# Performance work log

Measured on AMD Instinct MI355X. Metric: run time of the kernel, lower is better.

Reference implementation:

```python
import jax, jax.numpy as jnp
import numpy as np

B, S, D = 2, 2048, 1024
H = 16
DK = D // H
LW = 256          # local window size
GSTRIDE = 64      # global downsample stride
SW = 512          # sliding window size
EPS = 1e-5
SCALE = 1.0 / np.sqrt(DK)


def _layernorm(x, g, b):
    mu = jnp.mean(x, axis=-1, keepdims=True)
    var = jnp.mean(jnp.square(x - mu), axis=-1, keepdims=True)
    return (x - mu) * jax.lax.rsqrt(var + EPS) * g + b


def setup_inputs() -> dict:
    key = jax.random.key(0)
    ks = jax.random.split(key, 16)
    std = 0.02
    def lin(k, din, dout):
        kw, kb = jax.random.split(k)
        return (jax.random.normal(kw, (din, dout), jnp.float32) * std,
                jax.random.normal(kb, (dout,), jnp.float32) * std)
    inp = {}
    inp["x"] = jax.random.normal(ks[0], (B, S, D), jnp.float32)
    # hierarchical attention params
    inp["lq_w"], inp["lq_b"] = lin(ks[1], D, D)
    inp["lk_w"], inp["lk_b"] = lin(ks[2], D, D)
    inp["lv_w"], inp["lv_b"] = lin(ks[3], D, D)
    inp["gq_w"], inp["gq_b"] = lin(ks[4], D, D)
    inp["gk_w"], inp["gk_b"] = lin(ks[5], D, D)
    inp["gv_w"], inp["gv_b"] = lin(ks[6], D, D)
    inp["h_out_w"], inp["h_out_b"] = lin(ks[7], 2 * D, D)
    inp["h_ln_g"] = jnp.ones((D,), jnp.float32)
    inp["h_ln_b"] = jnp.zeros((D,), jnp.float32)
    # sliding window attention params
    inp["sq_w"], inp["sq_b"] = lin(ks[8], D, D)
    inp["sk_w"], inp["sk_b"] = lin(ks[9], D, D)
    inp["sv_w"], inp["sv_b"] = lin(ks[10], D, D)
    inp["s_out_w"], inp["s_out_b"] = lin(ks[11], D, D)
    # combination
    inp["comb_w"], inp["comb_b"] = lin(ks[12], 2 * D, D)
    inp["ln_g"] = jnp.ones((D,), jnp.float32)
    inp["ln_b"] = jnp.zeros((D,), jnp.float32)
    return inp


def _forward(x, lq_w, lq_b, lk_w, lk_b, lv_w, lv_b,
             gq_w, gq_b, gk_w, gk_b, gv_w, gv_b,
             h_out_w, h_out_b, h_ln_g, h_ln_b,
             sq_w, sq_b, sk_w, sk_b, sv_w, sv_b,
             s_out_w, s_out_b, comb_w, comb_b, ln_g, ln_b):
    nw = S // LW  # seq_len is a multiple of LW (no padding needed)

    # ---- Hierarchical: local windowed attention (vectorized over windows) ----
    xw = x.reshape(B, nw, LW, D)
    lq = (xw @ lq_w + lq_b).reshape(B, nw, LW, H, DK)
    lk = (xw @ lk_w + lk_b).reshape(B, nw, LW, H, DK)
    lv = (xw @ lv_w + lv_b).reshape(B, nw, LW, H, DK)
    lsc = jnp.einsum('bnqhd,bnkhd->bnhqk', lq, lk) * SCALE
    lat = jax.nn.softmax(lsc, axis=-1)
    local_out = jnp.einsum('bnhqk,bnkhd->bnqhd', lat, lv).reshape(B, S, D)

    # ---- Hierarchical: global attention over strided downsample ----
    gc = x[:, ::GSTRIDE]                 # [B, G, D], G = S // GSTRIDE
    G = gc.shape[1]
    gq = (x @ gq_w + gq_b).reshape(B, S, H, DK)
    gk = (gc @ gk_w + gk_b).reshape(B, G, H, DK)
    gv = (gc @ gv_w + gv_b).reshape(B, G, H, DK)
    gsc = jnp.einsum('bqhd,bkhd->bhqk', gq, gk) * SCALE
    gat = jax.nn.softmax(gsc, axis=-1)
    global_out = jnp.einsum('bhqk,bkhd->bqhd', gat, gv).reshape(B, S, D)

    h_comb = jnp.concatenate([local_out, global_out], axis=-1) @ h_out_w + h_out_b
    h_out = _layernorm(x + h_comb, h_ln_g, h_ln_b)

    # ---- Sliding window attention ----
    sq = (x @ sq_w + sq_b).reshape(B, S, H, DK)
    sk = (x @ sk_w + sk_b).reshape(B, S, H, DK)
    sv = (x @ sv_w + sv_b).reshape(B, S, H, DK)
    ssc = jnp.einsum('bqhd,bkhd->bhqk', sq, sk) * SCALE
    idx = jnp.arange(S)
    half = SW // 2
    band = jnp.abs(idx[:, None] - idx[None, :]) <= half   # [S, S]
    ssc = jnp.where(band[None, None], ssc, -jnp.inf)
    sat = jax.nn.softmax(ssc, axis=-1)
    s_attn = jnp.einsum('bhqk,bkhd->bqhd', sat, sv).reshape(B, S, D)
    s_out = s_attn @ s_out_w + s_out_b

    # ---- combine scales ----
    combined = jnp.concatenate([h_out, s_out], axis=-1) @ comb_w + comb_b
    return _layernorm(x + combined, ln_g, ln_b)


def reference(x, lq_w, lq_b, lk_w, lk_b, lv_w, lv_b,
              gq_w, gq_b, gk_w, gk_b, gv_w, gv_b,
              h_out_w, h_out_b, h_ln_g, h_ln_b,
              sq_w, sq_b, sk_w, sk_b, sv_w, sv_b,
              s_out_w, s_out_b, comb_w, comb_b, ln_g, ln_b):
    return _forward(x, lq_w, lq_b, lk_w, lk_b, lv_w, lv_b,
                    gq_w, gq_b, gk_w, gk_b, gv_w, gv_b,
                    h_out_w, h_out_b, h_ln_g, h_ln_b,
                    sq_w, sq_b, sk_w, sk_b, sv_w, sv_b,
                    s_out_w, s_out_b, comb_w, comb_b, ln_g, ln_b)
```

## Files before the change

kernel.cpp:

```cpp
#include <hip/hip_runtime.h>

#define BATCH 2
#define SEQ   2048
#define DIM   1024
#define NH    16
#define DK    64
#define SCALE_F 0.125f
#define MASKED  -2e30f
#define MINIT   -1e30f

typedef __attribute__((ext_vector_type(4))) float f4;
typedef __attribute__((ext_vector_type(4))) float f32x4;
typedef __attribute__((ext_vector_type(8))) short s16x8;
typedef __attribute__((ext_vector_type(4))) int  i32x4;
typedef __attribute__((ext_vector_type(4))) unsigned short u16x4;

__device__ __forceinline__ float bf2f(unsigned short u){ return __uint_as_float(((unsigned)u) << 16); }
__device__ __forceinline__ unsigned short f2bf(float f){
  unsigned u = __float_as_uint(f);
  u += 0x7FFFu + ((u >> 16) & 1u);
  return (unsigned short)(u >> 16);
}

#define ASYNC_LDS16(g, l) \
  __builtin_amdgcn_global_load_lds((const __attribute__((address_space(1))) void*)(g), \
                                   (__attribute__((address_space(3))) void*)(l), 16, 0, 0)

__global__ __launch_bounds__(256) void cast_bf16_kernel(const float* __restrict__ in,
                                                        unsigned short* __restrict__ out, int n){
  int i = (blockIdx.x * 256 + threadIdx.x) * 4;
  if (i < n){
    f4 v = *(const f4*)&in[i];
    u16x4 o = { f2bf(v[0]), f2bf(v[1]), f2bf(v[2]), f2bf(v[3]) };
    *(u16x4*)&out[i] = o;
  }
}

struct TCP { const float* w[12]; unsigned short* wt[12]; };
__global__ __launch_bounds__(256) void transpose_cast_b(TCP P, int K){
  const float* W = P.w[blockIdx.z];
  unsigned short* Wt = P.wt[blockIdx.z];
  __shared__ float tile[32][33];
  int x = threadIdx.x & 31, y = threadIdx.x >> 5;
  int bc = blockIdx.x << 5;
  int br = blockIdx.y << 5;
  #pragma unroll
  for (int yy = y; yy < 32; yy += 8)
    tile[yy][x] = W[(size_t)(br + yy) * DIM + bc + x];
  __syncthreads();
  #pragma unroll
  for (int yy = y; yy < 32; yy += 8)
    Wt[(size_t)(bc + yy) * K + br + x] = f2bf(tile[x][yy]);
}

__global__ __launch_bounds__(256) void gc_extract(const float* __restrict__ x,
                                                  unsigned short* __restrict__ gcb){
  int row = blockIdx.x;
  int t = threadIdx.x;
  unsigned short* dst = gcb + (size_t)row * DIM;
  if (row < BATCH * 32){
    int b = row >> 5, g = row & 31;
    const float* src = x + ((size_t)b * SEQ + (size_t)g * 64) * DIM;
    f4 v = *(const f4*)&src[t * 4];
    u16x4 o = { f2bf(v[0]), f2bf(v[1]), f2bf(v[2]), f2bf(v[3]) };
    *(u16x4*)&dst[t * 4] = o;
  } else {
    u16x4 z = { 0, 0, 0, 0 };
    *(u16x4*)&dst[t * 4] = z;
  }
}

struct GOut { unsigned short* ob; float* of; const float* bias; int ld; int tr; };
struct GOuts { GOut d[4]; };

template<int BN>
__global__ __launch_bounds__(256) void gemm_bf16(
    const unsigned short* __restrict__ A, const unsigned short* __restrict__ Bt,
    GOuts descs, int K)
{
  constexpr int NF = BN / 32;
  __shared__ __align__(16) unsigned short As[128 * 32];
  __shared__ __align__(16) unsigned short Bs[BN * 32];
  const int tid = threadIdx.x;
  const int lane = tid & 63;
  const int w = tid >> 6;
  const int wr = w >> 1, wc = w & 1;
  const int gx = gridDim.x;
  const int nwg = gx * gridDim.y;
  const int orig = blockIdx.y * gx + blockIdx.x;
  const int swz = (orig & 7) * (nwg >> 3) + (orig >> 3);
  const int tx = swz % gx, ty = swz / gx;
  const int tm = ty << 7, tn = tx * BN;
  const GOut dsc = descs.d[tn >> 10];
  const int trans = dsc.tr;

  const int r0 = tid >> 2;
  const int c0 = (tid & 3) << 3;
  const unsigned short* Ag0 = A + (size_t)(tm + r0) * K + c0;
  const unsigned short* Ag1 = A + (size_t)(tm + r0 + 64) * K + c0;
  const unsigned short* Bg0 = Bt + (size_t)(tn + r0) * K + c0;
  const unsigned short* Bg1 = Bt + (size_t)(tn + (BN == 128 ? r0 + 64 : r0)) * K + c0;
  unsigned short* AsW0 = &As[w * 512];
  unsigned short* AsW1 = &As[w * 512 + 2048];
  unsigned short* BsW0 = &Bs[w * 512];
  unsigned short* BsW1 = &Bs[(BN == 128 ? w * 512 + 2048 : w * 512)];

  f32x4 acc[4][NF];
  #pragma unroll
  for (int m = 0; m < 4; ++m)
    #pragma unroll
    for (int n = 0; n < NF; ++n) acc[m][n] = (f32x4){0.f, 0.f, 0.f, 0.f};

  const int fr = lane & 15, fg = lane >> 4;
  for (int kk = 0; kk < K; kk += 32){
    ASYNC_LDS16(Ag0 + kk, AsW0);
    ASYNC_LDS16(Ag1 + kk, AsW1);
    ASYNC_LDS16(Bg0 + kk, BsW0);
    if constexpr (BN == 128) ASYNC_LDS16(Bg1 + kk, BsW1);
    __syncthreads();
    s16x8 af[4], bfv[NF];
    #pragma unroll
    for (int m = 0; m < 4; ++m)
      af[m] = *(const s16x8*)&As[(wr * 64 + m * 16 + fr) * 32 + fg * 8];
    #pragma unroll
    for (int n = 0; n < NF; ++n)
      bfv[n] = *(const s16x8*)&Bs[(wc * (BN / 2) + n * 16 + fr) * 32 + fg * 8];
    if (trans){
      #pragma unroll
      for (int m = 0; m < 4; ++m)
        #pragma unroll
        for (int n = 0; n < NF; ++n)
          acc[m][n] = __builtin_amdgcn_mfma_f32_16x16x32_bf16(bfv[n], af[m], acc[m][n], 0, 0, 0);
    } else {
      #pragma unroll
      for (int m = 0; m < 4; ++m)
        #pragma unroll
        for (int n = 0; n < NF; ++n)
          acc[m][n] = __builtin_amdgcn_mfma_f32_16x16x32_bf16(af[m], bfv[n], acc[m][n], 0, 0, 0);
    }
    __syncthreads();
  }
  #pragma unroll
  for (int m = 0; m < 4; ++m){
    #pragma unroll
    for (int n = 0; n < NF; ++n){
      if (!trans){
        int cl = (tn + wc * (BN / 2) + n * 16 + fr) & 1023;
        float bv = dsc.bias ? dsc.bias[cl] : 0.f;
        #pragma unroll
        for (int r = 0; r < 4; ++r){
          int row = tm + wr * 64 + m * 16 + fg * 4 + r;
          float v = acc[m][n][r] + bv;
          if (dsc.of) dsc.of[(size_t)row * dsc.ld + cl] = v;
          if (dsc.ob) dsc.ob[(size_t)row * dsc.ld + cl] = f2bf(v);
        }
      } else {
        int colT = tm + wr * 64 + m * 16 + fr;
        #pragma unroll
        for (int r = 0; r < 4; ++r){
          int dl = (tn + wc * (BN / 2) + n * 16 + fg * 4 + r) & 1023;
          float v = acc[m][n][r] + (dsc.bias ? dsc.bias[dl] : 0.f);
          dsc.ob[(size_t)dl * dsc.ld + colT] = f2bf(v);
        }
      }
    }
  }
}

template<int MODE>
__global__ __launch_bounds__(256) void mfma_attn(
    const unsigned short* __restrict__ Qb,
    const unsigned short* __restrict__ Kb,
    const unsigned short* __restrict__ Vtb, int ldvt,
    unsigned short* __restrict__ Out, int ldo, int ocol)
{
  __shared__ __align__(16) unsigned short Ks[64][72];
  __shared__ __align__(16) unsigned short Vs[64][72];
  __shared__ __align__(16) unsigned short Pl[4][16][72];
  const int tid = threadIdx.x, lane = tid & 63, wv = tid >> 6;
  const int fr = lane & 15, fg = lane >> 4;
  const int blk = blockIdx.x;
  const int h  = blk & 15;
  const int qc = (blk >> 4) & 31;
  const int b  = blk >> 9;
  const int q0 = qc * 64;
  const int tq0 = b * SEQ + q0;
  int jlo, ntile;
  if (MODE == 0){ jlo = (qc >> 2) << 8; ntile = 4; }
  else if (MODE == 1){
    jlo = q0 - 256 < 0 ? 0 : q0 - 256;
    int jhi = q0 + 320 > SEQ ? SEQ : q0 + 320;
    ntile = (jhi - jlo) >> 6;
  } else { jlo = 0; ntile = 1; }
  const int ktok0 = (MODE == 2) ? b * 32 : b * SEQ;

  s16x8 qf[2];
  {
    const size_t qrow = (size_t)(tq0 + wv * 16 + fr) * DIM + h * DK;
    qf[0] = *(const s16x8*)&Qb[qrow + fg * 8];
    qf[1] = *(const s16x8*)&Qb[qrow + 32 + fg * 8];
  }
  f32x4 of[4];
  #pragma unroll
  for (int dt = 0; dt < 4; ++dt) of[dt] = (f32x4){0.f, 0.f, 0.f, 0.f};
  f32x4 m4 = (f32x4){MINIT, MINIT, MINIT, MINIT};
  f32x4 l4 = (f32x4){0.f, 0.f, 0.f, 0.f};

  for (int t = 0; t < ntile; ++t){
    const int jb = jlo + t * 64;
    __syncthreads();
    #pragma unroll
    for (int p = 0; p < 2; ++p){
      int idx = p * 256 + tid;
      int row = idx >> 3, c8 = idx & 7;
      *(i32x4*)&Ks[row][c8 * 8] =
          *(const i32x4*)&Kb[(size_t)(ktok0 + jb + row) * DIM + h * DK + c8 * 8];
      i32x4 v = *(const i32x4*)&Vtb[(size_t)(h * DK + row) * ldvt + ktok0 + jb + c8 * 8];
      *(i32x4*)((char*)Vs + row * 144 + ((c8 * 16) ^ ((row & 7) << 4))) = v;
    }
    __syncthreads();
    f32x4 sf[4];
    #pragma unroll
    for (int t16 = 0; t16 < 4; ++t16){
      sf[t16] = (f32x4){0.f, 0.f, 0.f, 0.f};
      #pragma unroll
      for (int ks = 0; ks < 2; ++ks){
        s16x8 kf = *(const s16x8*)&Ks[t16 * 16 + fr][ks * 32 + fg * 8];
        sf[t16] = __builtin_amdgcn_mfma_f32_16x16x32_bf16(qf[ks], kf, sf[t16], 0, 0, 0);
      }
    }
    #pragma unroll
    for (int t16 = 0; t16 < 4; ++t16){
      int j = jb + t16 * 16 + fr;
      #pragma unroll
      for (int r = 0; r < 4; ++r){
        float v = sf[t16][r] * SCALE_F;
        bool valid = true;
        if (MODE == 1){ int dq = (q0 + wv * 16 + fg * 4 + r) - j; valid = (dq <= 256) && (dq >= -256); }
        if (MODE == 2){ valid = j < 32; }
        sf[t16][r] = valid ? v : MASKED;
      }
    }
    f32x4 mx;
    #pragma unroll
    for (int r = 0; r < 4; ++r)
      mx[r] = fmaxf(fmaxf(sf[0][r], sf[1][r]), fmaxf(sf[2][r], sf[3][r]));
    #pragma unroll
    for (int off = 1; off < 16; off <<= 1){
      #pragma unroll
      for (int r = 0; r < 4; ++r) mx[r] = fmaxf(mx[r], __shfl_xor(mx[r], off));
    }
    f32x4 sc;
    #pragma unroll
    for (int r = 0; r < 4; ++r){
      float mn = fmaxf(m4[r], mx[r]);
      sc[r] = __expf(m4[r] - mn);
      m4[r] = mn;
    }
    f32x4 sm = (f32x4){0.f, 0.f, 0.f, 0.f};
    #pragma unroll
    for (int t16 = 0; t16 < 4; ++t16){
      #pragma unroll
      for (int r = 0; r < 4; ++r){
        float e = __expf(sf[t16][r] - m4[r]);
        sm[r] += e;
        Pl[wv][fg * 4 + r][t16 * 16 + fr] = f2bf(e);
      }
    }
    #pragma unroll
    for (int off = 1; off < 16; off <<= 1){
      #pragma unroll
      for (int r = 0; r < 4; ++r) sm[r] += __shfl_xor(sm[r], off);
    }
    #pragma unroll
    for (int r = 0; r < 4; ++r) l4[r] = l4[r] * sc[r] + sm[r];
    #pragma unroll
    for (int dt = 0; dt < 4; ++dt)
      #pragma unroll
      for (int r = 0; r < 4; ++r) of[dt][r] *= sc[r];
    #pragma unroll
    for (int ks2 = 0; ks2 < 2; ++ks2){
      s16x8 pa = *(const s16x8*)&Pl[wv][fr][ks2 * 32 + fg * 8];
      #pragma unroll
      for (int dt = 0; dt < 4; ++dt){
        int d = dt * 16 + fr;
        s16x8 vf = *(const s16x8*)((char*)Vs + d * 144 + ((ks2 * 64 + fg * 16) ^ ((d & 7) << 4)));
        of[dt] = __builtin_amdgcn_mfma_f32_16x16x32_bf16(pa, vf, of[dt], 0, 0, 0);
      }
    }
  }
  #pragma unroll
  for (int dt = 0; dt < 4; ++dt){
    #pragma unroll
    for (int r = 0; r < 4; ++r){
      float val = of[dt][r] / l4[r];
      int q = tq0 + wv * 16 + fg * 4 + r;
      Out[(size_t)q * ldo + ocol + h * DK + dt * 16 + fr] = f2bf(val);
    }
  }
}

__global__ __launch_bounds__(256) void ln_fused(
    const float* __restrict__ x, const float* __restrict__ dlt,
    const float* __restrict__ g, const float* __restrict__ bta,
    float* __restrict__ outf, unsigned short* __restrict__ outb, int ldo)
{
  const int row = blockIdx.x;
  const int t = threadIdx.x, lane = t & 63, wv = t >> 6;
  const float* xr = x + (size_t)row * DIM;
  const float* dr = dlt + (size_t)row * DIM;
  f4 xv = *(const f4*)&xr[t * 4];
  f4 dv = *(const f4*)&dr[t * 4];
  f4 y = xv + dv;
  float s = y[0] + y[1] + y[2] + y[3];
  float ss = y[0]*y[0] + y[1]*y[1] + y[2]*y[2] + y[3]*y[3];
  #pragma unroll
  for (int off = 1; off < 64; off <<= 1){ s += __shfl_xor(s, off); ss += __shfl_xor(ss, off); }
  __shared__ float red[8];
  if (lane == 0){ red[wv] = s; red[wv + 4] = ss; }
  __syncthreads();
  float S = red[0] + red[1] + red[2] + red[3];
  float SS = red[4] + red[5] + red[6] + red[7];
  float mu = S * (1.f / DIM);
  float var = SS * (1.f / DIM) - mu * mu;
  float rs = rsqrtf(var + 1e-5f);
  f4 gv = *(const f4*)&g[t * 4];
  f4 bv = *(const f4*)&bta[t * 4];
  f4 o;
  #pragma unroll
  for (int i = 0; i < 4; ++i) o[i] = (y[i] - mu) * rs * gv[i] + bv[i];
  if (outf) *(f4*)&outf[(size_t)row * ldo + t * 4] = o;
  if (outb){
    u16x4 ob = { f2bf(o[0]), f2bf(o[1]), f2bf(o[2]), f2bf(o[3]) };
    *(u16x4*)&outb[(size_t)row * ldo + t * 4] = ob;
  }
}

extern "C" void kernel_launch(void* const* d_in, const int* in_sizes, int n_in,
                              void* d_out, int out_size, void* d_ws, size_t ws_size,
                              hipStream_t stream){
  (void)in_sizes; (void)n_in; (void)out_size; (void)ws_size;
  const float* x      = (const float*)d_in[0];
  const float* lq_w   = (const float*)d_in[1];  const float* lq_b  = (const float*)d_in[2];
  const float* lk_w   = (const float*)d_in[3];  const float* lk_b  = (const float*)d_in[4];
  const float* lv_w   = (const float*)d_in[5];  const float* lv_b  = (const float*)d_in[6];
  const float* gq_w   = (const float*)d_in[7];  const float* gq_b  = (const float*)d_in[8];
  const float* gk_w   = (const float*)d_in[9];  const float* gk_b  = (const float*)d_in[10];
  const float* gv_w   = (const float*)d_in[11]; const float* gv_b  = (const float*)d_in[12];
  const float* ho_w   = (const float*)d_in[13]; const float* ho_b  = (const float*)d_in[14];
  const float* hln_g  = (const float*)d_in[15]; const float* hln_b = (const float*)d_in[16];
  const float* sq_w   = (const float*)d_in[17]; const float* sq_b  = (const float*)d_in[18];
  const float* sk_w   = (const float*)d_in[19]; const float* sk_b  = (const float*)d_in[20];
  const float* sv_w   = (const float*)d_in[21]; const float* sv_b  = (const float*)d_in[22];
  const float* so_w   = (const float*)d_in[23]; const float* so_b  = (const float*)d_in[24];
  const float* cb_w   = (const float*)d_in[25]; const float* cb_b  = (const float*)d_in[26];
  const float* ln_g   = (const float*)d_in[27]; const float* ln_b  = (const float*)d_in[28];

  const size_t M = (size_t)BATCH * SEQ;
  const size_t W1 = (size_t)DIM * DIM;
  char* ws = (char*)d_ws;
  size_t off = 0;
  auto alloc = [&](size_t bytes) -> void* {
    void* p = ws + off; off += (bytes + 255) & ~(size_t)255; return p;
  };
  unsigned short* xb    = (unsigned short*)alloc(M * DIM * 2);
  unsigned short* wt_s  = (unsigned short*)alloc(3 * W1 * 2);
  unsigned short* wt_lg = (unsigned short*)alloc(4 * W1 * 2);
  unsigned short* wt_g2 = (unsigned short*)alloc(2 * W1 * 2);
  unsigned short* wt_so = (unsigned short*)alloc(W1 * 2);
  unsigned short* wt_ho = (unsigned short*)alloc(2 * W1 * 2);
  unsigned short* wt_cb = (unsigned short*)alloc(2 * W1 * 2);
  unsigned short* gcb   = (unsigned short*)alloc((size_t)128 * DIM * 2);
  unsigned short* qb    = (unsigned short*)alloc(M * DIM * 2);
  unsigned short* kb    = (unsigned short*)alloc(M * DIM * 2);
  unsigned short* vtb   = (unsigned short*)alloc(M * DIM * 2);
  unsigned short* qg    = (unsigned short*)alloc(M * DIM * 2);
  unsigned short* gkb   = (unsigned short*)alloc((size_t)128 * DIM * 2);
  unsigned short* vtg   = (unsigned short*)alloc((size_t)128 * DIM * 2);
  unsigned short* satt  = (unsigned short*)alloc(M * DIM * 2);
  unsigned short* hcat  = (unsigned short*)alloc(M * 2 * DIM * 2);
  unsigned short* ccat  = (unsigned short*)alloc(M * 2 * DIM * 2);
  float* Af             = (float*)alloc(M * DIM * 4);

  dim3 b256(256);
  cast_bf16_kernel<<<dim3((M * DIM) / 1024), b256, 0, stream>>>(x, xb, (int)(M * DIM));
  {
    TCP p1 = {};
    const float* ws_[10] = {sq_w, sk_w, sv_w, lq_w, lk_w, lv_w, gq_w, gk_w, gv_w, so_w};
    unsigned short* wts_[10] = {wt_s, wt_s + W1, wt_s + 2 * W1,
                                wt_lg, wt_lg + W1, wt_lg + 2 * W1, wt_lg + 3 * W1,
                                wt_g2, wt_g2 + W1, wt_so};
    for (int i = 0; i < 10; ++i){ p1.w[i] = ws_[i]; p1.wt[i] = wts_[i]; }
    transpose_cast_b<<<dim3(32, 32, 10), b256, 0, stream>>>(p1, DIM);
    TCP p2 = {};
    p2.w[0] = ho_w; p2.wt[0] = wt_ho;
    p2.w[1] = cb_w; p2.wt[1] = wt_cb;
    transpose_cast_b<<<dim3(32, 64, 2), b256, 0, stream>>>(p2, 2 * DIM);
  }
  gc_extract<<<dim3(128), b256, 0, stream>>>(x, gcb);

  dim3 attn_grid(1024);
  auto mk = [&](unsigned short* ob, float* of, const float* bias, int ld, int tr) -> GOut {
    GOut g; g.ob = ob; g.of = of; g.bias = bias; g.ld = ld; g.tr = tr; return g;
  };

  {
    GOuts ds = {};
    ds.d[0] = mk(qb,  nullptr, sq_b, DIM, 0);
    ds.d[1] = mk(kb,  nullptr, sk_b, DIM, 0);
    ds.d[2] = mk(vtb, nullptr, sv_b, (int)M, 1);
    gemm_bf16<128><<<dim3(24, 32), b256, 0, stream>>>(xb, wt_s, ds, DIM);
  }
  mfma_attn<1><<<attn_grid, b256, 0, stream>>>(qb, kb, vtb, (int)M, satt, DIM, 0);

  {
    GOuts ds = {};
    ds.d[0] = mk(qb,  nullptr, lq_b, DIM, 0);
    ds.d[1] = mk(kb,  nullptr, lk_b, DIM, 0);
    ds.d[2] = mk(vtb, nullptr, lv_b, (int)M, 1);
    ds.d[3] = mk(qg,  nullptr, gq_b, DIM, 0);
    gemm_bf16<128><<<dim3(32, 32), b256, 0, stream>>>(xb, wt_lg, ds, DIM);
  }
  {
    GOuts ds = {};
    ds.d[0] = mk(ccat + 1024, nullptr, so_b, 2 * DIM, 0);
    gemm_bf16<64><<<dim3(16, 32), b256, 0, stream>>>(satt, wt_so, ds, DIM);
  }
  mfma_attn<0><<<attn_grid, b256, 0, stream>>>(qb, kb, vtb, (int)M, hcat, 2 * DIM, 0);

  {
    GOuts ds = {};
    ds.d[0] = mk(gkb, nullptr, gk_b, DIM, 0);
    ds.d[1] = mk(vtg, nullptr, gv_b, 128, 1);
    gemm_bf16<128><<<dim3(16, 1), b256, 0, stream>>>(gcb, wt_g2, ds, DIM);
  }
  mfma_attn<2><<<attn_grid, b256, 0, stream>>>(qg, gkb, vtg, 128, hcat, 2 * DIM, 1024);

  {
    GOuts ds = {};
    ds.d[0] = mk(nullptr, Af, ho_b, DIM, 0);
    gemm_bf16<64><<<dim3(16, 32), b256, 0, stream>>>(hcat, wt_ho, ds, 2 * DIM);
  }
  ln_fused<<<dim3((int)M), b256, 0, stream>>>(x, Af, hln_g, hln_b, nullptr, ccat, 2 * DIM);

  {
    GOuts ds = {};
    ds.d[0] = mk(nullptr, Af, cb_b, DIM, 0);
    gemm_bf16<64><<<dim3(16, 32), b256, 0, stream>>>(ccat, wt_cb, ds, 2 * DIM);
  }
  ln_fused<<<dim3((int)M), b256, 0, stream>>>(x, Af, ln_g, ln_b, (float*)d_out, nullptr, DIM);
}
```

Baseline: 565.2 us.

## Double-buffer GEMM LDS tiles with async prefetch and XOR-swizzled layout

The bf16 GEMM now uses two LDS buffers and prefetches the next two K-tiles with async global-to-LDS loads. It waits on explicit vmcnt counts, so loading tile t+2 overlaps the MFMA work on tile t instead of stalling at a barrier every iteration. It also XOR-swizzles the 16-byte K-chunk order per row pair so the fragment reads spread across LDS banks. The cost is twice the LDS footprint per block, which may lower occupancy, plus hand-written waitcnt and scheduling barriers that depend on how many loads each stage issues.

```diff
diff --git a/kernel.cpp b/kernel.cpp
--- a/kernel.cpp
+++ b/kernel.cpp
@@ -79,8 +79,8 @@
     GOuts descs, int K)
 {
   constexpr int NF = BN / 32;
-  __shared__ __align__(16) unsigned short As[128 * 32];
-  __shared__ __align__(16) unsigned short Bs[BN * 32];
+  __shared__ __align__(16) unsigned short As[2][128 * 32];
+  __shared__ __align__(16) unsigned short Bs[2][BN * 32];
   const int tid = threadIdx.x;
   const int lane = tid & 63;
   const int w = tid >> 6;
@@ -95,15 +95,11 @@
   const int trans = dsc.tr;
 
   const int r0 = tid >> 2;
-  const int c0 = (tid & 3) << 3;
-  const unsigned short* Ag0 = A + (size_t)(tm + r0) * K + c0;
-  const unsigned short* Ag1 = A + (size_t)(tm + r0 + 64) * K + c0;
-  const unsigned short* Bg0 = Bt + (size_t)(tn + r0) * K + c0;
-  const unsigned short* Bg1 = Bt + (size_t)(tn + (BN == 128 ? r0 + 64 : r0)) * K + c0;
-  unsigned short* AsW0 = &As[w * 512];
-  unsigned short* AsW1 = &As[w * 512 + 2048];
-  unsigned short* BsW0 = &Bs[w * 512];
-  unsigned short* BsW1 = &Bs[(BN == 128 ? w * 512 + 2048 : w * 512)];
+  const int ksw = (((tid & 3) ^ ((tid >> 3) & 3)) << 3);
+  const unsigned short* Ag0 = A + (size_t)(tm + r0) * K + ksw;
+  const unsigned short* Ag1 = A + (size_t)(tm + r0 + 64) * K + ksw;
+  const unsigned short* Bg0 = Bt + (size_t)(tn + r0) * K + ksw;
+  const unsigned short* Bg1 = Bt + (size_t)(tn + r0 + 64) * K + ksw;
 
   f32x4 acc[4][NF];
   #pragma unroll
@@ -112,19 +108,23 @@
     for (int n = 0; n < NF; ++n) acc[m][n] = (f32x4){0.f, 0.f, 0.f, 0.f};
 
   const int fr = lane & 15, fg = lane >> 4;
-  for (int kk = 0; kk < K; kk += 32){
-    ASYNC_LDS16(Ag0 + kk, AsW0);
-    ASYNC_LDS16(Ag1 + kk, AsW1);
-    ASYNC_LDS16(Bg0 + kk, BsW0);
-    if constexpr (BN == 128) ASYNC_LDS16(Bg1 + kk, BsW1);
-    __syncthreads();
+  const int kro = ((fg ^ ((fr >> 1) & 3)) << 3);
+
+  auto STAGE = [&](int buf, int t){
+    const int kk = t * 32;
+    ASYNC_LDS16(Ag0 + kk, &As[buf][w * 512]);
+    ASYNC_LDS16(Ag1 + kk, &As[buf][w * 512 + 2048]);
+    ASYNC_LDS16(Bg0 + kk, &Bs[buf][w * 512]);
+    if constexpr (BN == 128) ASYNC_LDS16(Bg1 + kk, &Bs[buf][w * 512 + 2048]);
+  };
+  auto COMPUTE = [&](int buf){
     s16x8 af[4], bfv[NF];
     #pragma unroll
     for (int m = 0; m < 4; ++m)
-      af[m] = *(const s16x8*)&As[(wr * 64 + m * 16 + fr) * 32 + fg * 8];
+      af[m] = *(const s16x8*)&As[buf][(wr * 64 + m * 16 + fr) * 32 + kro];
     #pragma unroll
     for (int n = 0; n < NF; ++n)
-      bfv[n] = *(const s16x8*)&Bs[(wc * (BN / 2) + n * 16 + fr) * 32 + fg * 8];
+      bfv[n] = *(const s16x8*)&Bs[buf][(wc * (BN / 2) + n * 16 + fr) * 32 + kro];
     if (trans){
       #pragma unroll
       for (int m = 0; m < 4; ++m)
@@ -138,8 +138,28 @@
         for (int n = 0; n < NF; ++n)
           acc[m][n] = __builtin_amdgcn_mfma_f32_16x16x32_bf16(af[m], bfv[n], acc[m][n], 0, 0, 0);
     }
-    __syncthreads();
-  }
+  };
+
+  const int nt = K >> 5;
+  STAGE(0, 0);
+  STAGE(1, 1);
+  for (int t = 0; t < nt - 1; ++t){
+    const int cur = t & 1;
+    if constexpr (BN == 128) asm volatile("s_waitcnt vmcnt(4)" ::: "memory");
+    else                     asm volatile("s_waitcnt vmcnt(3)" ::: "memory");
+    __builtin_amdgcn_s_barrier();
+    __builtin_amdgcn_sched_barrier(0);
+    COMPUTE(cur);
+    __builtin_amdgcn_sched_barrier(0);
+    __builtin_amdgcn_s_barrier();
+    __builtin_amdgcn_sched_barrier(0);
+    if (t + 2 < nt) STAGE(cur, t + 2);
+  }
+  asm volatile("s_waitcnt vmcnt(0)" ::: "memory");
+  __builtin_amdgcn_s_barrier();
+  __builtin_amdgcn_sched_barrier(0);
+  COMPUTE((nt - 1) & 1);
+
   #pragma unroll
   for (int m = 0; m < 4; ++m){
     #pragma unroll
```

Result: faster. 525.2 us (-7.1%).
